# Kernel tuning notes

Hardware: AMD Instinct MI355X
Metric: run time of the kernel (lower is better)

Reference implementation:

```python
import jax, jax.numpy as jnp
import numpy as np

EMBED_DIM = 512
NUM_JOINTS = 17
HIDDEN = EMBED_DIM * 2  # hidden_ratio=2
B, T = 32, 243


def setup_inputs() -> dict:
    key = jax.random.key(0)
    k_x, k_w1, k_w2 = jax.random.split(key, 3)
    x = jax.random.normal(k_x, (B, T, NUM_JOINTS, EMBED_DIM), dtype=jnp.float32)
    # kaiming_uniform with a=sqrt(5): bound = sqrt(6 / ((1 + a^2) * fan_in)) = sqrt(1/fan_in)
    b1 = float(np.sqrt(1.0 / EMBED_DIM))
    fc1_w = jax.random.uniform(k_w1, (NUM_JOINTS, EMBED_DIM, HIDDEN), minval=-b1, maxval=b1, dtype=jnp.float32)
    fc1_b = jnp.zeros((NUM_JOINTS, HIDDEN), dtype=jnp.float32)
    b2 = float(np.sqrt(1.0 / HIDDEN))
    fc2_w = jax.random.uniform(k_w2, (NUM_JOINTS, HIDDEN, 3), minval=-b2, maxval=b2, dtype=jnp.float32)
    fc2_b = jnp.zeros((NUM_JOINTS, 3), dtype=jnp.float32)
    ln_gamma = jnp.ones((EMBED_DIM,), dtype=jnp.float32)
    ln_beta = jnp.zeros((EMBED_DIM,), dtype=jnp.float32)
    return {"x": x, "ln_gamma": ln_gamma, "ln_beta": ln_beta,
            "fc1_w": fc1_w, "fc1_b": fc1_b, "fc2_w": fc2_w, "fc2_b": fc2_b}


def _layernorm(x, gamma, beta, eps=1e-5):
    mu = jnp.mean(x, axis=-1, keepdims=True)
    var = jnp.mean(jnp.square(x - mu), axis=-1, keepdims=True)
    return (x - mu) * jax.lax.rsqrt(var + eps) * gamma + beta


def reference(x, ln_gamma, ln_beta, fc1_w, fc1_b, fc2_w, fc2_b):
    # x: [B, T, J, d] -> [B, T, J, 3]
    xn = _layernorm(x, ln_gamma, ln_beta)
    h = jnp.einsum('btjd,jdh->btjh', xn, fc1_w) + fc1_b  # [B,T,J,H]
    h = jax.nn.gelu(h, approximate=False)  # torch GELU default is exact (erf)
    y = jnp.einsum('btjh,jho->btjo', h, fc2_w) + fc2_b  # [B,T,J,3]
    return y
```

## Files before the change

### kernel.cpp

```cpp
#include <hip/hip_runtime.h>
#include <hip/hip_bf16.h>

#define JN   17
#define DIM  512
#define HID  1024
#define MTOT 7776
#define MPAD 7936
#define NTHR 512

typedef __attribute__((ext_vector_type(8))) short s16x8;
typedef __attribute__((ext_vector_type(4))) float f32x4;
typedef unsigned short ushort_t;

__device__ __forceinline__ unsigned int f2bf(float f) {
    return (unsigned int)__builtin_bit_cast(unsigned short, __float2bfloat16(f));
}

__device__ __forceinline__ float gelu_erf(float h) {
    float ah = fabsf(h);
    float z  = ah * 0.7071067811865476f;
    float t  = __builtin_amdgcn_rcpf(fmaf(0.3275911f, z, 1.0f));
    float p  = fmaf(fmaf(fmaf(fmaf(1.061405429f, t, -1.453152027f), t,
                              1.421413741f), t, -0.284496736f), t, 0.254829592f);
    float er = 1.0f - p * t * __expf(-z * z);
    return fmaf(0.5f * ah, er, 0.5f * h);
}

__global__ __launch_bounds__(256)
void prep_w1(const float* __restrict__ w1, ushort_t* __restrict__ w1s) {
    int b  = blockIdx.x;
    int nq = b & 3;
    int kc = (b >> 2) & 15;
    int j  = b >> 6;
    int n  = nq * 256 + threadIdx.x;

    const float* src = w1 + ((size_t)j * DIM + kc * 32) * HID + n;
    ushort_t* dst = w1s + (((size_t)j * 16 + kc) * 1024 + n) * 32;

    #pragma unroll
    for (int u = 0; u < 4; ++u) {
        float v[8];
        #pragma unroll
        for (int e = 0; e < 8; ++e) v[e] = src[(u * 8 + e) * HID];
        uint4 qq;
        qq.x = f2bf(v[0]) | (f2bf(v[1]) << 16);
        qq.y = f2bf(v[2]) | (f2bf(v[3]) << 16);
        qq.z = f2bf(v[4]) | (f2bf(v[5]) << 16);
        qq.w = f2bf(v[6]) | (f2bf(v[7]) << 16);
        int p = u ^ ((n >> 1) & 3);
        *(uint4*)(dst + p * 8) = qq;
    }
}

__global__ __launch_bounds__(NTHR)
void prep_xn(const float* __restrict__ x,
             const float* __restrict__ gamma,
             const float* __restrict__ beta,
             ushort_t* __restrict__ xa)
{
    const int lane = threadIdx.x & 63;
    const int wv   = threadIdx.x >> 6;
    const int m    = blockIdx.x * 8 + wv;
    const int j    = blockIdx.y;

    const float4* gp = (const float4*)(gamma + lane * 8);
    const float4* bp = (const float4*)(beta + lane * 8);
    float4 g0 = gp[0], g1 = gp[1];
    float4 e0 = bp[0], e1 = bp[1];

    const float4* xp = (const float4*)(x + ((size_t)m * JN + j) * DIM + lane * 8);
    float4 va = xp[0], vb = xp[1];

    float s  = ((va.x + va.y) + (va.z + va.w)) + ((vb.x + vb.y) + (vb.z + vb.w));
    float s2 = fmaf(va.x, va.x, fmaf(va.y, va.y, fmaf(va.z, va.z, fmaf(va.w, va.w,
               fmaf(vb.x, vb.x, fmaf(vb.y, vb.y, fmaf(vb.z, vb.z, vb.w * vb.w)))))));
    #pragma unroll
    for (int d = 1; d < 64; d <<= 1) {
        s  += __shfl_xor(s,  d);
        s2 += __shfl_xor(s2, d);
    }
    float mu  = s * (1.0f / 512.0f);
    float var = s2 * (1.0f / 512.0f) - mu * mu;
    float rs  = rsqrtf(var + 1e-5f);

    float v0 = fmaf((va.x - mu) * rs, g0.x, e0.x);
    float v1 = fmaf((va.y - mu) * rs, g0.y, e0.y);
    float v2 = fmaf((va.z - mu) * rs, g0.z, e0.z);
    float v3 = fmaf((va.w - mu) * rs, g0.w, e0.w);
    float v4 = fmaf((vb.x - mu) * rs, g1.x, e1.x);
    float v5 = fmaf((vb.y - mu) * rs, g1.y, e1.y);
    float v6 = fmaf((vb.z - mu) * rs, g1.z, e1.z);
    float v7 = fmaf((vb.w - mu) * rs, g1.w, e1.w);
    uint4 qq;
    qq.x = f2bf(v0) | (f2bf(v1) << 16);
    qq.y = f2bf(v2) | (f2bf(v3) << 16);
    qq.z = f2bf(v4) | (f2bf(v5) << 16);
    qq.w = f2bf(v6) | (f2bf(v7) << 16);

    int kc = lane >> 2;
    *(uint4*)(xa + (((size_t)j * 16 + kc) * MPAD + m) * 32 + (lane & 3) * 8) = qq;
}

#define NWG11 (31 * 4 * JN)

__global__ __launch_bounds__(256, 3)
void pjh_gemm_v11(const ushort_t* __restrict__ xa,
                  const ushort_t* __restrict__ w1s,
                  const float* __restrict__ b1,
                  const float* __restrict__ w2,
                  float* __restrict__ ypart)
{
    __shared__ float Yp[4 * 64 * 3];
    const int tid  = threadIdx.x;
    const int lane = tid & 63;
    const int wn   = tid >> 6;

    const int q   = NWG11 / 8, r = NWG11 % 8;
    const int xcd = blockIdx.x & 7;
    const int lid = blockIdx.x >> 3;
    const int work = ((xcd < r) ? xcd * (q + 1) : r * (q + 1) + (xcd - r) * q) + lid;
    const int nt3  = work & 3;
    const int rest = work >> 2;
    const int mtg  = rest % 31;
    const int j    = rest / 31;

    const int kg = lane >> 4;
    const ushort_t* aB0 = xa + (size_t)j * 16 * MPAD * 32
                             + ((size_t)mtg * 256 + (lane & 15)) * 32 + kg * 8;
    const int pB = kg ^ (((lane & 15) >> 1) & 3);
    const ushort_t* bB0 = w1s + (size_t)j * 16 * 1024 * 32
                              + ((size_t)nt3 * 256 + wn * 64 + (lane & 15)) * 32 + pB * 8;

    float b1v[4], w20[4], w21[4], w22[4];
    #pragma unroll
    for (int nf = 0; nf < 4; ++nf) {
        int n = nt3 * 256 + wn * 64 + nf * 16 + (lane & 15);
        b1v[nf] = b1[j * HID + n];
        const float* w2p = w2 + ((size_t)j * HID + n) * 3;
        w20[nf] = w2p[0]; w21[nf] = w2p[1]; w22[nf] = w2p[2];
    }

    const ushort_t* aB = aB0;
    const ushort_t* bB = bB0;

#define LOADSET(FA, FB) do {                                                   \
        _Pragma("unroll")                                                      \
        for (int mf = 0; mf < 4; ++mf) FA[mf] = *(const s16x8*)(aB + mf * 512);\
        _Pragma("unroll")                                                      \
        for (int nf = 0; nf < 4; ++nf) FB[nf] = *(const s16x8*)(bB + nf * 512);\
        aB += (size_t)MPAD * 32;                                               \
        bB += 32768;                                                           \
    } while (0)

#define COMPUTE(FA, FB) do {                                                   \
        __builtin_amdgcn_s_setprio(1);                                         \
        _Pragma("unroll")                                                      \
        for (int mf = 0; mf < 4; ++mf)                                         \
            _Pragma("unroll")                                                  \
            for (int nf = 0; nf < 4; ++nf)                                     \
                acc[mf][nf] = __builtin_amdgcn_mfma_f32_16x16x32_bf16(FA[mf], FB[nf], acc[mf][nf], 0, 0, 0); \
        __builtin_amdgcn_s_setprio(0);                                         \
    } while (0)

    const f32x4 zero4 = {0.f, 0.f, 0.f, 0.f};
    f32x4 acc[4][4];
    #pragma unroll
    for (int mf = 0; mf < 4; ++mf)
        #pragma unroll
        for (int nf = 0; nf < 4; ++nf) acc[mf][nf] = zero4;

    s16x8 fA0[4], fB0[4], fA1[4], fB1[4];

    LOADSET(fA0, fB0);
    LOADSET(fA1, fB1);

    #pragma unroll 1
    for (int gg = 0; gg < 4; ++gg) {
        #pragma unroll 1
        for (int tp = 0; tp < 7; ++tp) {
            COMPUTE(fA0, fB0); LOADSET(fA0, fB0);
            COMPUTE(fA1, fB1); LOADSET(fA1, fB1);
        }
        COMPUTE(fA0, fB0);
        if (gg < 3) {
            aB = aB0 + (size_t)(gg + 1) * 2048;
            bB = bB0;
            LOADSET(fA0, fB0);
        }
        COMPUTE(fA1, fB1);
        if (gg < 3) {
            LOADSET(fA1, fB1);
        }

        #pragma unroll
        for (int mf = 0; mf < 4; ++mf) {
            #pragma unroll
            for (int rr = 0; rr < 4; ++rr) {
                float s0 = 0.f, s1 = 0.f, s2 = 0.f;
                #pragma unroll
                for (int nf = 0; nf < 4; ++nf) {
                    float gv = gelu_erf(acc[mf][nf][rr] + b1v[nf]);
                    s0 = fmaf(gv, w20[nf], s0);
                    s1 = fmaf(gv, w21[nf], s1);
                    s2 = fmaf(gv, w22[nf], s2);
                }
                s0 += __shfl_xor(s0, 1); s0 += __shfl_xor(s0, 2);
                s0 += __shfl_xor(s0, 4); s0 += __shfl_xor(s0, 8);
                s1 += __shfl_xor(s1, 1); s1 += __shfl_xor(s1, 2);
                s1 += __shfl_xor(s1, 4); s1 += __shfl_xor(s1, 8);
                s2 += __shfl_xor(s2, 1); s2 += __shfl_xor(s2, 2);
                s2 += __shfl_xor(s2, 4); s2 += __shfl_xor(s2, 8);
                if ((lane & 15) == 0) {
                    int m = mf * 16 + (lane >> 4) * 4 + rr;
                    Yp[(wn * 64 + m) * 3 + 0] = s0;
                    Yp[(wn * 64 + m) * 3 + 1] = s1;
                    Yp[(wn * 64 + m) * 3 + 2] = s2;
                }
            }
        }
        #pragma unroll
        for (int mf = 0; mf < 4; ++mf)
            #pragma unroll
            for (int nf = 0; nf < 4; ++nf) acc[mf][nf] = zero4;

        __syncthreads();
        for (int idx = tid; idx < 64 * 3; idx += 256) {
            int m = idx / 3;
            int o = idx - m * 3;
            int gr = mtg * 256 + gg * 64 + m;
            if (gr < MTOT) {
                float v = Yp[m * 3 + o] + Yp[(64 + m) * 3 + o]
                        + Yp[(128 + m) * 3 + o] + Yp[(192 + m) * 3 + o];
                ypart[(((size_t)nt3 * MPAD + gr) * JN + j) * 3 + o] = v;
            }
        }
        __syncthreads();
    }
#undef LOADSET
#undef COMPUTE
}

__global__ __launch_bounds__(512)
void fc2_reduce(const float* __restrict__ ypart,
                const float* __restrict__ b2,
                float* __restrict__ out)
{
    int idx = blockIdx.x * 512 + threadIdx.x;
    if (idx >= MTOT * JN * 3) return;
    int rest = idx / 3;
    int o = idx - rest * 3;
    int j = rest % JN;
    const size_t sl = (size_t)MPAD * JN * 3;
    float v = b2[j * 3 + o];
    #pragma unroll
    for (int s = 0; s < 4; ++s) v += ypart[s * sl + idx];
    out[idx] = v;
}

#define BM3 96
#define A3_OFF 0
#define B3_OFF 98304
#define Y3_OFF 98304
#define SMEM_V3 163840

__global__ __launch_bounds__(NTHR, 2)
void pjh_fused_v3(const float* __restrict__ x,
                  const float* __restrict__ gamma,
                  const float* __restrict__ beta,
                  const ushort_t* __restrict__ w1s,
                  const float* __restrict__ b1,
                  const float* __restrict__ w2,
                  const float* __restrict__ b2,
                  float* __restrict__ out)
{
    extern __shared__ char smem[];
    const int tid  = threadIdx.x;
    const int lane = tid & 63;
    const int wv   = tid >> 6;
    const int wm   = wv >> 2;
    const int wn   = wv & 3;
    const int mt   = blockIdx.x;
    const int j    = blockIdx.y;

    const ushort_t* w1j = w1s + (size_t)j * 16 * 1024 * 32;

    #pragma unroll
    for (int tt = 0; tt < 2; ++tt) {
        const ushort_t* tb = w1j + (size_t)tt * 1024 * 32;
        #pragma unroll
        for (int qq = 0; qq < 2; ++qq) {
            const ushort_t* src = tb + (size_t)(wv * 2 + qq) * 512 + lane * 8;
            void* dst = smem + B3_OFF + tt * 16384 + (wv * 2 + qq) * 1024;
            __builtin_amdgcn_global_load_lds(
                (const __attribute__((address_space(1))) unsigned int*)src,
                (__attribute__((address_space(3))) unsigned int*)dst, 16, 0, 0);
        }
    }

    {
        const float4* gp  = (const float4*)(gamma + lane * 8);
        const float4* bpp = (const float4*)(beta + lane * 8);
        float4 g0 = gp[0], g1 = gp[1];
        float4 e0 = bpp[0], e1 = bpp[1];
        #pragma unroll
        for (int rb = 0; rb < 12; rb += 4) {
            float4 xs[4][2];
            #pragma unroll
            for (int rr = 0; rr < 4; ++rr) {
                int gr = mt * BM3 + wv * 12 + rb + rr;
                const float4* xp = (const float4*)(x + ((size_t)gr * JN + j) * DIM + lane * 8);
                xs[rr][0] = xp[0]; xs[rr][1] = xp[1];
            }
            #pragma unroll
            for (int rr = 0; rr < 4; ++rr) {
                int m = wv * 12 + rb + rr;
                float4 va = xs[rr][0], vb = xs[rr][1];
                float s  = ((va.x + va.y) + (va.z + va.w)) + ((vb.x + vb.y) + (vb.z + vb.w));
                float s2 = fmaf(va.x, va.x, fmaf(va.y, va.y, fmaf(va.z, va.z, fmaf(va.w, va.w,
                           fmaf(vb.x, vb.x, fmaf(vb.y, vb.y, fmaf(vb.z, vb.z, vb.w * vb.w)))))));
                #pragma unroll
                for (int d = 1; d < 64; d <<= 1) {
                    s  += __shfl_xor(s,  d);
                    s2 += __shfl_xor(s2, d);
                }
                float mu  = s * (1.0f / 512.0f);
                float var = s2 * (1.0f / 512.0f) - mu * mu;
                float rs  = rsqrtf(var + 1e-5f);
                float v0 = fmaf((va.x - mu) * rs, g0.x, e0.x);
                float v1 = fmaf((va.y - mu) * rs, g0.y, e0.y);
                float v2 = fmaf((va.z - mu) * rs, g0.z, e0.z);
                float v3 = fmaf((va.w - mu) * rs, g0.w, e0.w);
                float v4 = fmaf((vb.x - mu) * rs, g1.x, e1.x);
                float v5 = fmaf((vb.y - mu) * rs, g1.y, e1.y);
                float v6 = fmaf((vb.z - mu) * rs, g1.z, e1.z);
                float v7 = fmaf((vb.w - mu) * rs, g1.w, e1.w);
                uint4 qq;
                qq.x = f2bf(v0) | (f2bf(v1) << 16);
                qq.y = f2bf(v2) | (f2bf(v3) << 16);
                qq.z = f2bf(v4) | (f2bf(v5) << 16);
                qq.w = f2bf(v6) | (f2bf(v7) << 16);
                *(uint4*)(smem + A3_OFF + m * 1024 + ((lane ^ (m & 7)) * 16)) = qq;
            }
        }
    }

    __syncthreads();

    float yr[3][4][3];
    #pragma unroll
    for (int a = 0; a < 3; ++a)
        #pragma unroll
        for (int rr = 0; rr < 4; ++rr)
            #pragma unroll
            for (int o = 0; o < 3; ++o) yr[a][rr][o] = 0.f;

    const f32x4 zero4 = {0.f, 0.f, 0.f, 0.f};
    f32x4 acc[3][4];
    #pragma unroll
    for (int mf = 0; mf < 3; ++mf)
        #pragma unroll
        for (int nf = 0; nf < 4; ++nf) acc[mf][nf] = zero4;

    #pragma unroll 1
    for (int t = 0; t < 64; ++t) {
        if (t + 2 < 64) {
            int kc = (t + 2) & 15, nt = (t + 2) >> 4;
            const ushort_t* tb = w1j + ((size_t)kc * 1024 + nt * 256) * 32;
            int bb = ((t + 2) & 3) * 16384;
            #pragma unroll
            for (int qq = 0; qq < 2; ++qq) {
                const ushort_t* src = tb + (size_t)(wv * 2 + qq) * 512 + lane * 8;
                void* dst = smem + B3_OFF + bb + (wv * 2 + qq) * 1024;
                __builtin_amdgcn_global_load_lds(
                    (const __attribute__((address_space(1))) unsigned int*)src,
                    (__attribute__((address_space(3))) unsigned int*)dst, 16, 0, 0);
            }
        }

        int kc = t & 15;
        int bb = (t & 3) * 16384;
        int g  = lane >> 4;
        s16x8 aF[3], bF[4];
        #pragma unroll
        for (int mf = 0; mf < 3; ++mf) {
            int m  = wm * 48 + mf * 16 + (lane & 15);
            int ul = kc * 4 + g;
            aF[mf] = *(const s16x8*)(smem + A3_OFF + m * 1024 + ((ul ^ (m & 7)) * 16));
        }
        #pragma unroll
        for (int nf = 0; nf < 4; ++nf) {
            int nl = wn * 64 + nf * 16 + (lane & 15);
            int p  = g ^ ((nl >> 1) & 3);
            bF[nf] = *(const s16x8*)(smem + B3_OFF + bb + (nl * 4 + p) * 16);
        }

        __builtin_amdgcn_s_setprio(1);
        #pragma unroll
        for (int mf = 0; mf < 3; ++mf)
            #pragma unroll
            for (int nf = 0; nf < 4; ++nf)
                acc[mf][nf] = __builtin_amdgcn_mfma_f32_16x16x32_bf16(aF[mf], bF[nf], acc[mf][nf], 0, 0, 0);
        __builtin_amdgcn_s_setprio(0);

        if ((t & 15) == 15) {
            int nt = t >> 4;
            #pragma unroll
            for (int nf = 0; nf < 4; ++nf) {
                int n = nt * 256 + wn * 64 + nf * 16 + (lane & 15);
                float b1v = b1[j * HID + n];
                const float* w2p = w2 + ((size_t)j * HID + n) * 3;
                float w20 = w2p[0], w21 = w2p[1], w22 = w2p[2];
                #pragma unroll
                for (int mf = 0; mf < 3; ++mf) {
                    #pragma unroll
                    for (int rr = 0; rr < 4; ++rr) {
                        float gv = gelu_erf(acc[mf][nf][rr] + b1v);
                        yr[mf][rr][0] = fmaf(gv, w20, yr[mf][rr][0]);
                        yr[mf][rr][1] = fmaf(gv, w21, yr[mf][rr][1]);
                        yr[mf][rr][2] = fmaf(gv, w22, yr[mf][rr][2]);
                    }
                }
            }
            #pragma unroll
            for (int mf = 0; mf < 3; ++mf)
                #pragma unroll
                for (int nf = 0; nf < 4; ++nf)
                    acc[mf][nf] = zero4;
        }

        if (t < 62) {
            asm volatile("s_waitcnt vmcnt(2)" ::: "memory");
        } else {
            asm volatile("s_waitcnt vmcnt(0)" ::: "memory");
        }
        __builtin_amdgcn_s_barrier();
    }

    #pragma unroll
    for (int mf = 0; mf < 3; ++mf)
        #pragma unroll
        for (int rr = 0; rr < 4; ++rr)
            #pragma unroll
            for (int o = 0; o < 3; ++o) {
                float v = yr[mf][rr][o];
                v += __shfl_xor(v, 1);
                v += __shfl_xor(v, 2);
                v += __shfl_xor(v, 4);
                v += __shfl_xor(v, 8);
                yr[mf][rr][o] = v;
            }

    __syncthreads();

    float* Yp = (float*)(smem + Y3_OFF);
    if ((lane & 15) == 0) {
        int mrow = lane >> 4;
        #pragma unroll
        for (int mf = 0; mf < 3; ++mf)
            #pragma unroll
            for (int rr = 0; rr < 4; ++rr) {
                int m = wm * 48 + mf * 16 + mrow * 4 + rr;
                #pragma unroll
                for (int o = 0; o < 3; ++o)
                    Yp[(wn * BM3 + m) * 3 + o] = yr[mf][rr][o];
            }
    }
    __syncthreads();

    if (tid < BM3 * 3) {
        int m = tid / 3;
        int o = tid - m * 3;
        int gr = mt * BM3 + m;
        float v = Yp[m * 3 + o] + Yp[(BM3 + m) * 3 + o]
                + Yp[(2 * BM3 + m) * 3 + o] + Yp[(3 * BM3 + m) * 3 + o]
                + b2[j * 3 + o];
        out[((size_t)gr * JN + j) * 3 + o] = v;
    }
}

extern "C" void kernel_launch(void* const* d_in, const int* in_sizes, int n_in,
                              void* d_out, int out_size, void* d_ws, size_t ws_size,
                              hipStream_t stream) {
    (void)in_sizes; (void)n_in; (void)out_size;
    const float* x   = (const float*)d_in[0];
    const float* ga  = (const float*)d_in[1];
    const float* be  = (const float*)d_in[2];
    const float* w1  = (const float*)d_in[3];
    const float* b1  = (const float*)d_in[4];
    const float* w2  = (const float*)d_in[5];
    const float* b2  = (const float*)d_in[6];
    float* out = (float*)d_out;

    const size_t xa_bytes  = (size_t)JN * 16 * MPAD * 32 * sizeof(ushort_t);
    const size_t w1s_bytes = (size_t)JN * 16 * 1024 * 32 * sizeof(ushort_t);
    const size_t yp_bytes  = (size_t)4 * MPAD * JN * 3 * sizeof(float);

    if (ws_size >= xa_bytes + w1s_bytes + yp_bytes) {
        ushort_t* xa  = (ushort_t*)d_ws;
        ushort_t* w1s = (ushort_t*)((char*)d_ws + xa_bytes);
        float* ypart  = (float*)((char*)d_ws + xa_bytes + w1s_bytes);
        prep_xn<<<dim3(MTOT / 8, JN), NTHR, 0, stream>>>(x, ga, be, xa);
        prep_w1<<<JN * 16 * 4, 256, 0, stream>>>(w1, w1s);
        pjh_gemm_v11<<<NWG11, 256, 0, stream>>>(xa, w1s, b1, w2, ypart);
        fc2_reduce<<<(MTOT * JN * 3 + 511) / 512, 512, 0, stream>>>(ypart, b2, out);
    } else {
        ushort_t* w1s = (ushort_t*)d_ws;
        prep_w1<<<JN * 16 * 4, 256, 0, stream>>>(w1, w1s);
        hipFuncSetAttribute((const void*)pjh_fused_v3,
                            hipFuncAttributeMaxDynamicSharedMemorySize, SMEM_V3);
        dim3 grid(MTOT / BM3, JN);
        pjh_fused_v3<<<grid, NTHR, SMEM_V3, stream>>>(x, ga, be, w1s, b1, w2, b2, out);
    }
}
```

Measured before the change: 349.1 us.

## Stage GEMM tiles through LDS with async global-to-LDS DMA double buffering

Replaces the register-direct global-load GEMM with a 512-thread, 8-wave kernel that stages 256x256xK tiles into double-buffered 128KB LDS using global_load_lds DMA. Each wave computes a 128x64 subtile with A-fragments shared across N waves, so each global element is loaded once per workgroup instead of once per wave. The xa layout gets an XOR swizzle to avoid LDS bank conflicts. In exchange it needs per-phase barriers, large LDS (limiting occupancy) and 128 accumulator registers per wave.

Measured after the change: 379.2 us. 8.6% more time.

```diff
diff --git a/kernel.cpp b/kernel.cpp
--- a/kernel.cpp
+++ b/kernel.cpp
@@ -98,38 +98,131 @@
     qq.w = f2bf(v6) | (f2bf(v7) << 16);
 
     int kc = lane >> 2;
-    *(uint4*)(xa + (((size_t)j * 16 + kc) * MPAD + m) * 32 + (lane & 3) * 8) = qq;
-}
-
-#define NWG11 (31 * 4 * JN)
-
-__global__ __launch_bounds__(256, 3)
-void pjh_gemm_v11(const ushort_t* __restrict__ xa,
+    int p  = (lane & 3) ^ (m & 3) ^ ((m >> 2) & 3);
+    *(uint4*)(xa + (((size_t)j * 16 + kc) * MPAD + m) * 32 + p * 8) = qq;
+}
+
+#define SMEM_V12 131072
+#define NWG12 (31 * 4 * JN)
+
+__global__ __launch_bounds__(NTHR, 2)
+void pjh_gemm_v12(const ushort_t* __restrict__ xa,
                   const ushort_t* __restrict__ w1s,
                   const float* __restrict__ b1,
                   const float* __restrict__ w2,
                   float* __restrict__ ypart)
 {
-    __shared__ float Yp[4 * 64 * 3];
+    extern __shared__ char smem[];
     const int tid  = threadIdx.x;
     const int lane = tid & 63;
-    const int wn   = tid >> 6;
-
-    const int q   = NWG11 / 8, r = NWG11 % 8;
+    const int wv   = tid >> 6;
+    const int wm   = wv >> 2;
+    const int wn   = wv & 3;
+
+    const int q   = NWG12 / 8, r = NWG12 % 8;
     const int xcd = blockIdx.x & 7;
     const int lid = blockIdx.x >> 3;
     const int work = ((xcd < r) ? xcd * (q + 1) : r * (q + 1) + (xcd - r) * q) + lid;
     const int nt3  = work & 3;
     const int rest = work >> 2;
-    const int mtg  = rest % 31;
+    const int mt   = rest % 31;
     const int j    = rest / 31;
 
-    const int kg = lane >> 4;
-    const ushort_t* aB0 = xa + (size_t)j * 16 * MPAD * 32
-                             + ((size_t)mtg * 256 + (lane & 15)) * 32 + kg * 8;
-    const int pB = kg ^ (((lane & 15) >> 1) & 3);
-    const ushort_t* bB0 = w1s + (size_t)j * 16 * 1024 * 32
-                              + ((size_t)nt3 * 256 + wn * 64 + (lane & 15)) * 32 + pB * 8;
+    const char* xaJ = (const char*)xa  + (size_t)j * 16 * MPAD * 64 + (size_t)mt * 16384;
+    const char* w1J = (const char*)w1s + (size_t)j * 16 * 65536   + (size_t)nt3 * 16384;
+    const size_t xaK = (size_t)MPAD * 64;
+
+    int aoff[8];
+    #pragma unroll
+    for (int mf = 0; mf < 8; ++mf) {
+        int ml = wm * 128 + mf * 16 + (lane & 15);
+        int p  = (lane >> 4) ^ (ml & 3) ^ ((ml >> 2) & 3);
+        aoff[mf] = ml * 64 + p * 16;
+    }
+    int boff[4];
+    {
+        int pB = (lane >> 4) ^ (((lane & 15) >> 1) & 3);
+        #pragma unroll
+        for (int nf = 0; nf < 4; ++nf) {
+            int nl = wn * 64 + nf * 16 + (lane & 15);
+            boff[nf] = 32768 + nl * 64 + pB * 16;
+        }
+    }
+
+    const int cA = wv * 1024 + lane * 16;
+
+#define DMA(SRC, DST) __builtin_amdgcn_global_load_lds(                         \
+        (const __attribute__((address_space(1))) unsigned int*)(SRC),           \
+        (__attribute__((address_space(3))) unsigned int*)(DST), 16, 0, 0)
+
+#define STAGE(KT, BN) do {                                                      \
+        const char* sa0 = xaJ + (size_t)(2*(KT))   * xaK + cA;                  \
+        const char* sa1 = xaJ + (size_t)(2*(KT)+1) * xaK + cA;                  \
+        const char* sb0 = w1J + (size_t)(2*(KT))   * 65536 + cA;                \
+        const char* sb1 = w1J + (size_t)(2*(KT)+1) * 65536 + cA;                \
+        DMA(sa0,        smem + (BN) + cA);                                      \
+        DMA(sa0 + 8192, smem + (BN) + 8192  + cA);                              \
+        DMA(sa1,        smem + (BN) + 16384 + cA);                              \
+        DMA(sa1 + 8192, smem + (BN) + 16384 + 8192 + cA);                       \
+        DMA(sb0,        smem + (BN) + 32768 + cA);                              \
+        DMA(sb0 + 8192, smem + (BN) + 32768 + 8192 + cA);                       \
+        DMA(sb1,        smem + (BN) + 49152 + cA);                              \
+        DMA(sb1 + 8192, smem + (BN) + 49152 + 8192 + cA);                       \
+    } while (0)
+
+#define PHASE(MB, BC) do {                                                      \
+        s16x8 aF0 = *(const s16x8*)(smem + (BC) + aoff[MB]);                    \
+        s16x8 aF1 = *(const s16x8*)(smem + (BC) + aoff[MB] + 16384);            \
+        s16x8 aF2 = *(const s16x8*)(smem + (BC) + aoff[MB + 1]);                \
+        s16x8 aF3 = *(const s16x8*)(smem + (BC) + aoff[MB + 1] + 16384);        \
+        __builtin_amdgcn_s_barrier();                                           \
+        __builtin_amdgcn_s_setprio(1);                                          \
+        _Pragma("unroll")                                                       \
+        for (int nf = 0; nf < 4; ++nf) {                                        \
+            acc[MB][nf]     = __builtin_amdgcn_mfma_f32_16x16x32_bf16(aF0, bF0[nf], acc[MB][nf], 0, 0, 0);     \
+            acc[MB][nf]     = __builtin_amdgcn_mfma_f32_16x16x32_bf16(aF1, bF1[nf], acc[MB][nf], 0, 0, 0);     \
+            acc[MB + 1][nf] = __builtin_amdgcn_mfma_f32_16x16x32_bf16(aF2, bF0[nf], acc[MB + 1][nf], 0, 0, 0); \
+            acc[MB + 1][nf] = __builtin_amdgcn_mfma_f32_16x16x32_bf16(aF3, bF1[nf], acc[MB + 1][nf], 0, 0, 0); \
+        }                                                                       \
+        __builtin_amdgcn_s_setprio(0);                                          \
+        __builtin_amdgcn_s_barrier();                                           \
+    } while (0)
+
+    const f32x4 zero4 = {0.f, 0.f, 0.f, 0.f};
+    f32x4 acc[8][4];
+    #pragma unroll
+    for (int mf = 0; mf < 8; ++mf)
+        #pragma unroll
+        for (int nf = 0; nf < 4; ++nf) acc[mf][nf] = zero4;
+
+    STAGE(0, 0);
+    asm volatile("s_waitcnt vmcnt(0)" ::: "memory");
+    __builtin_amdgcn_s_barrier();
+
+    #pragma unroll 1
+    for (int kt = 0; kt < 8; ++kt) {
+        const int bc = (kt & 1) * 65536;
+        const int bn = bc ^ 65536;
+
+        s16x8 bF0[4], bF1[4];
+        #pragma unroll
+        for (int nf = 0; nf < 4; ++nf) {
+            bF0[nf] = *(const s16x8*)(smem + bc + boff[nf]);
+            bF1[nf] = *(const s16x8*)(smem + bc + boff[nf] + 16384);
+        }
+        if (kt < 7) STAGE(kt + 1, bn);
+
+        PHASE(0, bc);
+        PHASE(2, bc);
+        PHASE(4, bc);
+        PHASE(6, bc);
+
+        asm volatile("s_waitcnt vmcnt(0)" ::: "memory");
+        __builtin_amdgcn_s_barrier();
+    }
+
+    __syncthreads();
+    float* Yp = (float*)smem;
 
     float b1v[4], w20[4], w21[4], w22[4];
     #pragma unroll
@@ -140,104 +233,47 @@
         w20[nf] = w2p[0]; w21[nf] = w2p[1]; w22[nf] = w2p[2];
     }
 
-    const ushort_t* aB = aB0;
-    const ushort_t* bB = bB0;
-
-#define LOADSET(FA, FB) do {                                                   \
-        _Pragma("unroll")                                                      \
-        for (int mf = 0; mf < 4; ++mf) FA[mf] = *(const s16x8*)(aB + mf * 512);\
-        _Pragma("unroll")                                                      \
-        for (int nf = 0; nf < 4; ++nf) FB[nf] = *(const s16x8*)(bB + nf * 512);\
-        aB += (size_t)MPAD * 32;                                               \
-        bB += 32768;                                                           \
-    } while (0)
-
-#define COMPUTE(FA, FB) do {                                                   \
-        __builtin_amdgcn_s_setprio(1);                                         \
-        _Pragma("unroll")                                                      \
-        for (int mf = 0; mf < 4; ++mf)                                         \
-            _Pragma("unroll")                                                  \
-            for (int nf = 0; nf < 4; ++nf)                                     \
-                acc[mf][nf] = __builtin_amdgcn_mfma_f32_16x16x32_bf16(FA[mf], FB[nf], acc[mf][nf], 0, 0, 0); \
-        __builtin_amdgcn_s_setprio(0);                                         \
-    } while (0)
-
-    const f32x4 zero4 = {0.f, 0.f, 0.f, 0.f};
-    f32x4 acc[4][4];
-    #pragma unroll
-    for (int mf = 0; mf < 4; ++mf)
-        #pragma unroll
-        for (int nf = 0; nf < 4; ++nf) acc[mf][nf] = zero4;
-
-    s16x8 fA0[4], fB0[4], fA1[4], fB1[4];
-
-    LOADSET(fA0, fB0);
-    LOADSET(fA1, fB1);
-
-    #pragma unroll 1
-    for (int gg = 0; gg < 4; ++gg) {
-        #pragma unroll 1
-        for (int tp = 0; tp < 7; ++tp) {
-            COMPUTE(fA0, fB0); LOADSET(fA0, fB0);
-            COMPUTE(fA1, fB1); LOADSET(fA1, fB1);
-        }
-        COMPUTE(fA0, fB0);
-        if (gg < 3) {
-            aB = aB0 + (size_t)(gg + 1) * 2048;
-            bB = bB0;
-            LOADSET(fA0, fB0);
-        }
-        COMPUTE(fA1, fB1);
-        if (gg < 3) {
-            LOADSET(fA1, fB1);
-        }
-
-        #pragma unroll
-        for (int mf = 0; mf < 4; ++mf) {
-            #pragma unroll
-            for (int rr = 0; rr < 4; ++rr) {
-                float s0 = 0.f, s1 = 0.f, s2 = 0.f;
-                #pragma unroll
-                for (int nf = 0; nf < 4; ++nf) {
-                    float gv = gelu_erf(acc[mf][nf][rr] + b1v[nf]);
-                    s0 = fmaf(gv, w20[nf], s0);
-                    s1 = fmaf(gv, w21[nf], s1);
-                    s2 = fmaf(gv, w22[nf], s2);
-                }
-                s0 += __shfl_xor(s0, 1); s0 += __shfl_xor(s0, 2);
-                s0 += __shfl_xor(s0, 4); s0 += __shfl_xor(s0, 8);
-                s1 += __shfl_xor(s1, 1); s1 += __shfl_xor(s1, 2);
-                s1 += __shfl_xor(s1, 4); s1 += __shfl_xor(s1, 8);
-                s2 += __shfl_xor(s2, 1); s2 += __shfl_xor(s2, 2);
-                s2 += __shfl_xor(s2, 4); s2 += __shfl_xor(s2, 8);
-                if ((lane & 15) == 0) {
-                    int m = mf * 16 + (lane >> 4) * 4 + rr;
-                    Yp[(wn * 64 + m) * 3 + 0] = s0;
-                    Yp[(wn * 64 + m) * 3 + 1] = s1;
-                    Yp[(wn * 64 + m) * 3 + 2] = s2;
-                }
-            }
-        }
-        #pragma unroll
-        for (int mf = 0; mf < 4; ++mf)
-            #pragma unroll
-            for (int nf = 0; nf < 4; ++nf) acc[mf][nf] = zero4;
-
-        __syncthreads();
-        for (int idx = tid; idx < 64 * 3; idx += 256) {
-            int m = idx / 3;
-            int o = idx - m * 3;
-            int gr = mtg * 256 + gg * 64 + m;
-            if (gr < MTOT) {
-                float v = Yp[m * 3 + o] + Yp[(64 + m) * 3 + o]
-                        + Yp[(128 + m) * 3 + o] + Yp[(192 + m) * 3 + o];
-                ypart[(((size_t)nt3 * MPAD + gr) * JN + j) * 3 + o] = v;
-            }
-        }
-        __syncthreads();
-    }
-#undef LOADSET
-#undef COMPUTE
+    #pragma unroll
+    for (int mf = 0; mf < 8; ++mf) {
+        #pragma unroll
+        for (int rr = 0; rr < 4; ++rr) {
+            float s0 = 0.f, s1 = 0.f, s2 = 0.f;
+            #pragma unroll
+            for (int nf = 0; nf < 4; ++nf) {
+                float gv = gelu_erf(acc[mf][nf][rr] + b1v[nf]);
+                s0 = fmaf(gv, w20[nf], s0);
+                s1 = fmaf(gv, w21[nf], s1);
+                s2 = fmaf(gv, w22[nf], s2);
+            }
+            s0 += __shfl_xor(s0, 1); s0 += __shfl_xor(s0, 2);
+            s0 += __shfl_xor(s0, 4); s0 += __shfl_xor(s0, 8);
+            s1 += __shfl_xor(s1, 1); s1 += __shfl_xor(s1, 2);
+            s1 += __shfl_xor(s1, 4); s1 += __shfl_xor(s1, 8);
+            s2 += __shfl_xor(s2, 1); s2 += __shfl_xor(s2, 2);
+            s2 += __shfl_xor(s2, 4); s2 += __shfl_xor(s2, 8);
+            if ((lane & 15) == 0) {
+                int m = wm * 128 + mf * 16 + (lane >> 4) * 4 + rr;
+                Yp[(wn * 256 + m) * 3 + 0] = s0;
+                Yp[(wn * 256 + m) * 3 + 1] = s1;
+                Yp[(wn * 256 + m) * 3 + 2] = s2;
+            }
+        }
+    }
+    __syncthreads();
+
+    for (int idx = tid; idx < 256 * 3; idx += NTHR) {
+        int m = idx / 3;
+        int o = idx - m * 3;
+        int gr = mt * 256 + m;
+        if (gr < MTOT) {
+            float v = Yp[(m) * 3 + o] + Yp[(256 + m) * 3 + o]
+                    + Yp[(512 + m) * 3 + o] + Yp[(768 + m) * 3 + o];
+            ypart[(((size_t)nt3 * MPAD + gr) * JN + j) * 3 + o] = v;
+        }
+    }
+#undef DMA
+#undef STAGE
+#undef PHASE
 }
 
 __global__ __launch_bounds__(512)
@@ -501,7 +537,9 @@
         float* ypart  = (float*)((char*)d_ws + xa_bytes + w1s_bytes);
         prep_xn<<<dim3(MTOT / 8, JN), NTHR, 0, stream>>>(x, ga, be, xa);
         prep_w1<<<JN * 16 * 4, 256, 0, stream>>>(w1, w1s);
-        pjh_gemm_v11<<<NWG11, 256, 0, stream>>>(xa, w1s, b1, w2, ypart);
+        hipFuncSetAttribute((const void*)pjh_gemm_v12,
+                            hipFuncAttributeMaxDynamicSharedMemorySize, SMEM_V12);
+        pjh_gemm_v12<<<NWG12, NTHR, SMEM_V12, stream>>>(xa, w1s, b1, w2, ypart);
         fc2_reduce<<<(MTOT * JN * 3 + 511) / 512, 512, 0, stream>>>(ypart, b2, out);
     } else {
         ushort_t* w1s = (ushort_t*)d_ws;
```

## Stage GEMM tiles through LDS with async global-to-LDS DMA and 128x128 tiles

Applied to the files above, without the earlier changes.

Replaces the register-direct global loads of the per-joint GEMM with double-buffered LDS staging using global_load_lds DMA. Tiles change from 256x256 per workgroup (4 waves along N) to 128x128 (2x2 waves), so each wave's A and B fragments are shared through LDS rather than each wave fetching its own. The xa layout gains an XOR swizzle to avoid LDS bank conflicts, and MPAD shrinks to fit 128-row tiles. N is now split into 8 partials instead of 4, which doubles the partial-sum traffic that fc2_reduce reads, and each K step adds a barrier.

New measurement: 310.3 us. 11.1% less time.

```diff
diff --git a/kernel.cpp b/kernel.cpp
--- a/kernel.cpp
+++ b/kernel.cpp
@@ -5,7 +5,7 @@
 #define DIM  512
 #define HID  1024
 #define MTOT 7776
-#define MPAD 7936
+#define MPAD 7808
 #define NTHR 512
 
 typedef __attribute__((ext_vector_type(8))) short s16x8;
@@ -98,146 +98,159 @@
     qq.w = f2bf(v6) | (f2bf(v7) << 16);
 
     int kc = lane >> 2;
-    *(uint4*)(xa + (((size_t)j * 16 + kc) * MPAD + m) * 32 + (lane & 3) * 8) = qq;
-}
-
-#define NWG11 (31 * 4 * JN)
+    int p  = (lane & 3) ^ (m & 3) ^ ((m >> 2) & 3);
+    *(uint4*)(xa + (((size_t)j * 16 + kc) * MPAD + m) * 32 + p * 8) = qq;
+}
+
+#define SMEM_V13 32768
+#define NWG13 (61 * 8 * JN)
 
 __global__ __launch_bounds__(256, 3)
-void pjh_gemm_v11(const ushort_t* __restrict__ xa,
+void pjh_gemm_v13(const ushort_t* __restrict__ xa,
                   const ushort_t* __restrict__ w1s,
                   const float* __restrict__ b1,
                   const float* __restrict__ w2,
                   float* __restrict__ ypart)
 {
-    __shared__ float Yp[4 * 64 * 3];
+    extern __shared__ char smem[];
     const int tid  = threadIdx.x;
     const int lane = tid & 63;
-    const int wn   = tid >> 6;
-
-    const int q   = NWG11 / 8, r = NWG11 % 8;
-    const int xcd = blockIdx.x & 7;
-    const int lid = blockIdx.x >> 3;
-    const int work = ((xcd < r) ? xcd * (q + 1) : r * (q + 1) + (xcd - r) * q) + lid;
-    const int nt3  = work & 3;
-    const int rest = work >> 2;
-    const int mtg  = rest % 31;
-    const int j    = rest / 31;
-
-    const int kg = lane >> 4;
-    const ushort_t* aB0 = xa + (size_t)j * 16 * MPAD * 32
-                             + ((size_t)mtg * 256 + (lane & 15)) * 32 + kg * 8;
-    const int pB = kg ^ (((lane & 15) >> 1) & 3);
-    const ushort_t* bB0 = w1s + (size_t)j * 16 * 1024 * 32
-                              + ((size_t)nt3 * 256 + wn * 64 + (lane & 15)) * 32 + pB * 8;
+    const int wv   = tid >> 6;
+    const int wm   = wv >> 1;
+    const int wn   = wv & 1;
+
+    const int xcd  = blockIdx.x & 7;
+    const int lid  = blockIdx.x >> 3;
+    const int work = xcd * (NWG13 / 8) + lid;
+    const int nt2  = work & 7;
+    const int rest = work >> 3;
+    const int mt   = rest % 61;
+    const int j    = rest / 61;
+
+    const char* xaJ = (const char*)xa  + (size_t)j * 16 * MPAD * 64 + (size_t)mt * 8192;
+    const char* w1J = (const char*)w1s + (size_t)j * 16 * 65536   + (size_t)nt2 * 8192;
+    const size_t xaK = (size_t)MPAD * 64;
+
+    const int g = lane >> 4;
+    int aoff[4], boff[4];
+    #pragma unroll
+    for (int mf = 0; mf < 4; ++mf) {
+        int ml = wm * 64 + mf * 16 + (lane & 15);
+        int p  = g ^ (ml & 3) ^ ((ml >> 2) & 3);
+        aoff[mf] = ml * 64 + p * 16;
+    }
+    {
+        int pB = g ^ (((lane & 15) >> 1) & 3);
+        #pragma unroll
+        for (int nf = 0; nf < 4; ++nf) {
+            int nl = wn * 64 + nf * 16 + (lane & 15);
+            int p  = g ^ ((nl >> 1) & 3);
+            boff[nf] = 8192 + nl * 64 + p * 16;
+        }
+        (void)pB;
+    }
+
+    const int cT = tid * 16;
+
+#define DMA(SRC, DST) __builtin_amdgcn_global_load_lds(                         \
+        (const __attribute__((address_space(1))) unsigned int*)(SRC),           \
+        (__attribute__((address_space(3))) unsigned int*)(DST), 16, 0, 0)
+
+#define STAGE(KC, BN) do {                                                      \
+        const char* sa = xaJ + (size_t)(KC) * xaK + cT;                         \
+        const char* sb = w1J + (size_t)(KC) * 65536 + cT;                       \
+        DMA(sa,        smem + (BN) + cT);                                       \
+        DMA(sa + 4096, smem + (BN) + 4096 + cT);                                \
+        DMA(sb,        smem + (BN) + 8192 + cT);                                \
+        DMA(sb + 4096, smem + (BN) + 8192 + 4096 + cT);                         \
+    } while (0)
+
+#define STEP(BN) do {                                                           \
+        s16x8 aF[4], bF[4];                                                     \
+        _Pragma("unroll")                                                       \
+        for (int mf = 0; mf < 4; ++mf)                                          \
+            aF[mf] = *(const s16x8*)(smem + (BN) + aoff[mf]);                   \
+        _Pragma("unroll")                                                       \
+        for (int nf = 0; nf < 4; ++nf)                                          \
+            bF[nf] = *(const s16x8*)(smem + (BN) + boff[nf]);                   \
+        __builtin_amdgcn_s_setprio(1);                                          \
+        _Pragma("unroll")                                                       \
+        for (int mf = 0; mf < 4; ++mf)                                          \
+            _Pragma("unroll")                                                   \
+            for (int nf = 0; nf < 4; ++nf)                                      \
+                acc[mf][nf] = __builtin_amdgcn_mfma_f32_16x16x32_bf16(aF[mf], bF[nf], acc[mf][nf], 0, 0, 0); \
+        __builtin_amdgcn_s_setprio(0);                                          \
+    } while (0)
+
+    const f32x4 zero4 = {0.f, 0.f, 0.f, 0.f};
+    f32x4 acc[4][4];
+    #pragma unroll
+    for (int mf = 0; mf < 4; ++mf)
+        #pragma unroll
+        for (int nf = 0; nf < 4; ++nf) acc[mf][nf] = zero4;
+
+    STAGE(0, 0);
+    __syncthreads();
+
+    #pragma unroll 1
+    for (int t = 0; t < 16; ++t) {
+        int bc = (t & 1) * 16384;
+        if (t + 1 < 16) STAGE(t + 1, bc ^ 16384);
+        STEP(bc);
+        __syncthreads();
+    }
+
+    float* Yp = (float*)smem;
 
     float b1v[4], w20[4], w21[4], w22[4];
     #pragma unroll
     for (int nf = 0; nf < 4; ++nf) {
-        int n = nt3 * 256 + wn * 64 + nf * 16 + (lane & 15);
+        int n = nt2 * 128 + wn * 64 + nf * 16 + (lane & 15);
         b1v[nf] = b1[j * HID + n];
         const float* w2p = w2 + ((size_t)j * HID + n) * 3;
         w20[nf] = w2p[0]; w21[nf] = w2p[1]; w22[nf] = w2p[2];
     }
 
-    const ushort_t* aB = aB0;
-    const ushort_t* bB = bB0;
-
-#define LOADSET(FA, FB) do {                                                   \
-        _Pragma("unroll")                                                      \
-        for (int mf = 0; mf < 4; ++mf) FA[mf] = *(const s16x8*)(aB + mf * 512);\
-        _Pragma("unroll")                                                      \
-        for (int nf = 0; nf < 4; ++nf) FB[nf] = *(const s16x8*)(bB + nf * 512);\
-        aB += (size_t)MPAD * 32;                                               \
-        bB += 32768;                                                           \
-    } while (0)
-
-#define COMPUTE(FA, FB) do {                                                   \
-        __builtin_amdgcn_s_setprio(1);                                         \
-        _Pragma("unroll")                                                      \
-        for (int mf = 0; mf < 4; ++mf)                                         \
-            _Pragma("unroll")                                                  \
-            for (int nf = 0; nf < 4; ++nf)                                     \
-                acc[mf][nf] = __builtin_amdgcn_mfma_f32_16x16x32_bf16(FA[mf], FB[nf], acc[mf][nf], 0, 0, 0); \
-        __builtin_amdgcn_s_setprio(0);                                         \
-    } while (0)
-
-    const f32x4 zero4 = {0.f, 0.f, 0.f, 0.f};
-    f32x4 acc[4][4];
-    #pragma unroll
-    for (int mf = 0; mf < 4; ++mf)
-        #pragma unroll
-        for (int nf = 0; nf < 4; ++nf) acc[mf][nf] = zero4;
-
-    s16x8 fA0[4], fB0[4], fA1[4], fB1[4];
-
-    LOADSET(fA0, fB0);
-    LOADSET(fA1, fB1);
-
-    #pragma unroll 1
-    for (int gg = 0; gg < 4; ++gg) {
-        #pragma unroll 1
-        for (int tp = 0; tp < 7; ++tp) {
-            COMPUTE(fA0, fB0); LOADSET(fA0, fB0);
-            COMPUTE(fA1, fB1); LOADSET(fA1, fB1);
-        }
-        COMPUTE(fA0, fB0);
-        if (gg < 3) {
-            aB = aB0 + (size_t)(gg + 1) * 2048;
-            bB = bB0;
-            LOADSET(fA0, fB0);
-        }
-        COMPUTE(fA1, fB1);
-        if (gg < 3) {
-            LOADSET(fA1, fB1);
-        }
-
-        #pragma unroll
-        for (int mf = 0; mf < 4; ++mf) {
-            #pragma unroll
-            for (int rr = 0; rr < 4; ++rr) {
-                float s0 = 0.f, s1 = 0.f, s2 = 0.f;
-                #pragma unroll
-                for (int nf = 0; nf < 4; ++nf) {
-                    float gv = gelu_erf(acc[mf][nf][rr] + b1v[nf]);
-                    s0 = fmaf(gv, w20[nf], s0);
-                    s1 = fmaf(gv, w21[nf], s1);
-                    s2 = fmaf(gv, w22[nf], s2);
-                }
-                s0 += __shfl_xor(s0, 1); s0 += __shfl_xor(s0, 2);
-                s0 += __shfl_xor(s0, 4); s0 += __shfl_xor(s0, 8);
-                s1 += __shfl_xor(s1, 1); s1 += __shfl_xor(s1, 2);
-                s1 += __shfl_xor(s1, 4); s1 += __shfl_xor(s1, 8);
-                s2 += __shfl_xor(s2, 1); s2 += __shfl_xor(s2, 2);
-                s2 += __shfl_xor(s2, 4); s2 += __shfl_xor(s2, 8);
-                if ((lane & 15) == 0) {
-                    int m = mf * 16 + (lane >> 4) * 4 + rr;
-                    Yp[(wn * 64 + m) * 3 + 0] = s0;
-                    Yp[(wn * 64 + m) * 3 + 1] = s1;
-                    Yp[(wn * 64 + m) * 3 + 2] = s2;
-                }
-            }
-        }
-        #pragma unroll
-        for (int mf = 0; mf < 4; ++mf)
-            #pragma unroll
-            for (int nf = 0; nf < 4; ++nf) acc[mf][nf] = zero4;
-
-        __syncthreads();
-        for (int idx = tid; idx < 64 * 3; idx += 256) {
-            int m = idx / 3;
-            int o = idx - m * 3;
-            int gr = mtg * 256 + gg * 64 + m;
-            if (gr < MTOT) {
-                float v = Yp[m * 3 + o] + Yp[(64 + m) * 3 + o]
-                        + Yp[(128 + m) * 3 + o] + Yp[(192 + m) * 3 + o];
-                ypart[(((size_t)nt3 * MPAD + gr) * JN + j) * 3 + o] = v;
-            }
-        }
-        __syncthreads();
-    }
-#undef LOADSET
-#undef COMPUTE
+    #pragma unroll
+    for (int mf = 0; mf < 4; ++mf) {
+        #pragma unroll
+        for (int rr = 0; rr < 4; ++rr) {
+            float s0 = 0.f, s1 = 0.f, s2 = 0.f;
+            #pragma unroll
+            for (int nf = 0; nf < 4; ++nf) {
+                float gv = gelu_erf(acc[mf][nf][rr] + b1v[nf]);
+                s0 = fmaf(gv, w20[nf], s0);
+                s1 = fmaf(gv, w21[nf], s1);
+                s2 = fmaf(gv, w22[nf], s2);
+            }
+            s0 += __shfl_xor(s0, 1); s0 += __shfl_xor(s0, 2);
+            s0 += __shfl_xor(s0, 4); s0 += __shfl_xor(s0, 8);
+            s1 += __shfl_xor(s1, 1); s1 += __shfl_xor(s1, 2);
+            s1 += __shfl_xor(s1, 4); s1 += __shfl_xor(s1, 8);
+            s2 += __shfl_xor(s2, 1); s2 += __shfl_xor(s2, 2);
+            s2 += __shfl_xor(s2, 4); s2 += __shfl_xor(s2, 8);
+            if ((lane & 15) == 0) {
+                int m = wm * 64 + mf * 16 + (lane >> 4) * 4 + rr;
+                Yp[(wn * 128 + m) * 3 + 0] = s0;
+                Yp[(wn * 128 + m) * 3 + 1] = s1;
+                Yp[(wn * 128 + m) * 3 + 2] = s2;
+            }
+        }
+    }
+    __syncthreads();
+
+    for (int idx = tid; idx < 128 * 3; idx += 256) {
+        int m = idx / 3;
+        int o = idx - m * 3;
+        int gr = mt * 128 + m;
+        if (gr < MTOT) {
+            float v = Yp[m * 3 + o] + Yp[(128 + m) * 3 + o];
+            ypart[(((size_t)nt2 * MPAD + gr) * JN + j) * 3 + o] = v;
+        }
+    }
+#undef DMA
+#undef STAGE
+#undef STEP
 }
 
 __global__ __launch_bounds__(512)
@@ -253,7 +266,7 @@
     const size_t sl = (size_t)MPAD * JN * 3;
     float v = b2[j * 3 + o];
     #pragma unroll
-    for (int s = 0; s < 4; ++s) v += ypart[s * sl + idx];
+    for (int s = 0; s < 8; ++s) v += ypart[s * sl + idx];
     out[idx] = v;
 }
 
@@ -493,7 +506,7 @@
 
     const size_t xa_bytes  = (size_t)JN * 16 * MPAD * 32 * sizeof(ushort_t);
     const size_t w1s_bytes = (size_t)JN * 16 * 1024 * 32 * sizeof(ushort_t);
-    const size_t yp_bytes  = (size_t)4 * MPAD * JN * 3 * sizeof(float);
+    const size_t yp_bytes  = (size_t)8 * MPAD * JN * 3 * sizeof(float);
 
     if (ws_size >= xa_bytes + w1s_bytes + yp_bytes) {
         ushort_t* xa  = (ushort_t*)d_ws;
@@ -501,7 +514,9 @@
         float* ypart  = (float*)((char*)d_ws + xa_bytes + w1s_bytes);
         prep_xn<<<dim3(MTOT / 8, JN), NTHR, 0, stream>>>(x, ga, be, xa);
         prep_w1<<<JN * 16 * 4, 256, 0, stream>>>(w1, w1s);
-        pjh_gemm_v11<<<NWG11, 256, 0, stream>>>(xa, w1s, b1, w2, ypart);
+        hipFuncSetAttribute((const void*)pjh_gemm_v13,
+                            hipFuncAttributeMaxDynamicSharedMemorySize, SMEM_V13);
+        pjh_gemm_v13<<<NWG13, 256, SMEM_V13, stream>>>(xa, w1s, b1, w2, ypart);
         fc2_reduce<<<(MTOT * JN * 3 + 511) / 512, 512, 0, stream>>>(ypart, b2, out);
     } else {
         ushort_t* w1s = (ushort_t*)d_ws;
```
